# Optimization experiments

Hardware: AMD Instinct MI355X
Metric: run time of the kernel (lower is better)

## Reference

```python
import jax, jax.numpy as jnp
import numpy as np

B, T, D, H = 8, 2048, 1024, 128  # batch, seq (== block_size), n_embd, head_size


def setup_inputs() -> dict:
    key = jax.random.key(0)
    kx, kq, kk, kv = jax.random.split(key, 4)
    s = D ** -0.5  # rough linear-init scale
    return {
        "x": jax.random.normal(kx, (B, T, D), dtype=jnp.float32),
        "Wq": jax.random.normal(kq, (D, H), dtype=jnp.float32) * s,
        "Wk": jax.random.normal(kk, (D, H), dtype=jnp.float32) * s,
        "Wv": jax.random.normal(kv, (D, H), dtype=jnp.float32) * s,
    }


def reference(x, Wq, Wk, Wv):
    # Linear projections (no bias)
    q = x @ Wq  # [B, T, H]
    k = x @ Wk  # [B, T, H]
    v = x @ Wv  # [B, T, H]
    scale = k.shape[-1] ** -0.5
    scores = jnp.einsum("bth,bsh->bts", q, k) * scale  # [B, T, T]
    # causal mask from tril buffer
    causal = jnp.tril(jnp.ones((T, T), dtype=bool))
    scores = jnp.where(causal, scores, jnp.finfo(scores.dtype).min)
    att = jax.nn.softmax(scores, axis=-1)
    out = jnp.einsum("bts,bsh->bth", att, v)  # [B, T, H]
    return out
```

## Files before the change

kernel.cpp:

```cpp
#include <hip/hip_runtime.h>
#include <hip/hip_bf16.h>
#include <stdint.h>

typedef float f32x4 __attribute__((ext_vector_type(4)));
typedef __bf16 bf16x8 __attribute__((ext_vector_type(8)));

#define T_SEQ 2048
#define D_EMB 1024
#define H_DIM 128
#define NBATCH 8
#define NTOK 16384

typedef __attribute__((address_space(3))) uint32_t lds_u32;
typedef const __attribute__((address_space(1))) uint32_t glb_u32;

#define DPPF(x, ctrl)                                                    \
  __int_as_float(__builtin_amdgcn_update_dpp(                            \
      0, __float_as_int(x), (ctrl), 0xF, 0xF, true))

#define PIPE_FENCE()                                       \
  do {                                                     \
    asm volatile("s_waitcnt vmcnt(0)" ::: "memory");       \
    __builtin_amdgcn_s_barrier();                          \
    __builtin_amdgcn_sched_barrier(0);                     \
  } while (0)


__global__ __launch_bounds__(256) void prep_w_kernel(
    const float* __restrict__ Wq, const float* __restrict__ Wk,
    const float* __restrict__ Wv, __hip_bfloat16* __restrict__ Wt) {
  const int mat = blockIdx.x >> 7;
  const int h = blockIdx.x & 127;
  const float* W = (mat == 0) ? Wq : ((mat == 1) ? Wk : Wv);
  __hip_bfloat16* dst = Wt + (size_t)(mat * 128 + h) * D_EMB;
  for (int k = threadIdx.x; k < D_EMB; k += 256)
    dst[k] = __float2bfloat16(W[(size_t)k * H_DIM + h]);
}

__global__ __launch_bounds__(512) void proj_kernel(
    const float* __restrict__ x, const __hip_bfloat16* __restrict__ Wt,
    __hip_bfloat16* __restrict__ qb, __hip_bfloat16* __restrict__ kb,
    __hip_bfloat16* __restrict__ vt) {
  __shared__ __align__(16) float Af[2][64 * 64];
  __shared__ __align__(16) __hip_bfloat16 Bs[2][384 * 64];
  const int tid = threadIdx.x;
  const int wave = tid >> 6;
  const int lane = tid & 63;
  const int g = lane >> 4;
  const int lr = lane & 15;
  const int m0 = blockIdx.x * 64;
  const int wc = wave * 48;

  f32x4 acc[4][3];
#pragma unroll
  for (int m = 0; m < 4; ++m)
#pragma unroll
    for (int n = 0; n < 3; ++n) acc[m][n] = f32x4{0.f, 0.f, 0.f, 0.f};

  auto stageA = [&](int buf, int k0) {
#pragma unroll
    for (int i = 0; i < 2; ++i) {
      const int e = i * 512 + tid;
      const int row = e >> 4;
      const int un = e & 15;
      __builtin_amdgcn_global_load_lds(
          (glb_u32*)(uintptr_t)(x + (size_t)(m0 + row) * D_EMB + k0 +
                                ((un ^ (row & 15)) * 4)),
          (lds_u32*)(uintptr_t)(&Af[buf][e * 4]), 16, 0, 0);
    }
  };
  auto stageB = [&](int buf, int k0) {
#pragma unroll
    for (int i = 0; i < 6; ++i) {
      const int u = i * 512 + tid;
      const int row = u >> 3;
      const int chunk = u & 7;
      __builtin_amdgcn_global_load_lds(
          (glb_u32*)(uintptr_t)(Wt + (size_t)row * D_EMB + k0 +
                                ((chunk ^ (row & 7)) * 8)),
          (lds_u32*)(uintptr_t)(&Bs[buf][row * 64 + chunk * 8]), 16, 0, 0);
    }
  };
  auto compute = [&](int buf) {
#pragma unroll
    for (int kk = 0; kk < 2; ++kk) {
      bf16x8 a[4];
#pragma unroll
      for (int m = 0; m < 4; ++m) {
        const int row = m * 16 + lr;
        const int u0 = kk * 8 + g * 2;
        const f32x4 lo = *reinterpret_cast<const f32x4*>(
            &Af[buf][row * 64 + ((u0 ^ (row & 15)) * 4)]);
        const f32x4 hi = *reinterpret_cast<const f32x4*>(
            &Af[buf][row * 64 + (((u0 + 1) ^ (row & 15)) * 4)]);
        union { bf16x8 v; __hip_bfloat16 h[8]; } u;
        u.h[0] = __float2bfloat16(lo[0]);
        u.h[1] = __float2bfloat16(lo[1]);
        u.h[2] = __float2bfloat16(lo[2]);
        u.h[3] = __float2bfloat16(lo[3]);
        u.h[4] = __float2bfloat16(hi[0]);
        u.h[5] = __float2bfloat16(hi[1]);
        u.h[6] = __float2bfloat16(hi[2]);
        u.h[7] = __float2bfloat16(hi[3]);
        a[m] = u.v;
      }
#pragma unroll
      for (int n = 0; n < 3; ++n) {
        const int row = wc + n * 16 + lr;
        bf16x8 b = *reinterpret_cast<const bf16x8*>(
            &Bs[buf][row * 64 + (((kk * 4 + g) ^ (row & 7)) * 8)]);
#pragma unroll
        for (int m = 0; m < 4; ++m)
          acc[m][n] =
              __builtin_amdgcn_mfma_f32_16x16x32_bf16(a[m], b, acc[m][n], 0, 0, 0);
      }
    }
  };

  stageA(0, 0);
  stageB(0, 0);

  int cur = 0;
  for (int k = 0; k < 16; ++k) {
    PIPE_FENCE();
    if (k < 15) {
      stageA(cur ^ 1, (k + 1) * 64);
      stageB(cur ^ 1, (k + 1) * 64);
    }
    compute(cur);
    cur ^= 1;
  }

#pragma unroll
  for (int n = 0; n < 3; ++n) {
    const int ng = wc + n * 16 + lr;
    const int head = ng >> 7;
    const int h = ng & 127;
#pragma unroll
    for (int m = 0; m < 4; ++m) {
#pragma unroll
      for (int r = 0; r < 4; ++r) {
        const int row = m0 + m * 16 + g * 4 + r;
        const __hip_bfloat16 val = __float2bfloat16(acc[m][n][r]);
        if (head == 0) {
          qb[(size_t)row * H_DIM + h] = val;
        } else if (head == 1) {
          kb[(size_t)row * H_DIM + h] = val;
        } else {
          const int bi = row >> 11;
          const int t = row & (T_SEQ - 1);
          vt[((size_t)bi * H_DIM + h) * T_SEQ + t] = val;
        }
      }
    }
  }
}

__global__ __launch_bounds__(512) void attn_kernel(
    const __hip_bfloat16* __restrict__ qb, const __hip_bfloat16* __restrict__ kb,
    const __hip_bfloat16* __restrict__ vt, float* __restrict__ out,
    float* __restrict__ PA_O, float* __restrict__ PA_ml,
    float* __restrict__ PB_O, float* __restrict__ PB_ml) {
  __shared__ __align__(16) __hip_bfloat16 KV[2][16384];
  __shared__ __align__(16) __hip_bfloat16 Pl[8][16][40];
  __shared__ float Obuf[4][16][132];
  __shared__ float mbuf[8][16];
  __shared__ float lbuf[8][16];

  const int tid = threadIdx.x;
  const int wave = tid >> 6;
  const int lane = tid & 63;
  const int g = lane >> 4;
  const int lr = lane & 15;
  const int qt = wave >> 1;
  const int kp = wave & 1;
  const int idx = blockIdx.x;
  const int b = idx & 7;
  const int u = idx >> 3;

  const __hip_bfloat16* qB = qb + (size_t)b * T_SEQ * H_DIM;
  const __hip_bfloat16* kB = kb + (size_t)b * T_SEQ * H_DIM;
  const __hip_bfloat16* vB = vt + (size_t)b * H_DIM * T_SEQ;
  const float scale = 0.08838834764831845f;

  auto stage = [&](__hip_bfloat16* buf, int s0) {
#pragma unroll
    for (int i = 0; i < 2; ++i) {
      const int uu = tid + i * 512;
      const int row = uu >> 4, grp = uu & 15;
      __builtin_amdgcn_global_load_lds(
          (glb_u32*)(uintptr_t)(kB + (size_t)(s0 + row) * H_DIM +
                                ((grp ^ (row & 15)) * 8)),
          (lds_u32*)(uintptr_t)(buf + uu * 8), 16, 0, 0);
    }
#pragma unroll
    for (int i = 0; i < 2; ++i) {
      const int uu = tid + i * 512;
      const int h = uu >> 3, grp = uu & 7;
      __builtin_amdgcn_global_load_lds(
          (glb_u32*)(uintptr_t)(vB + (size_t)h * T_SEQ + s0 +
                                ((grp ^ (h & 7)) * 8)),
          (lds_u32*)(uintptr_t)(buf + 8192 + uu * 8), 16, 0, 0);
    }
  };

  auto process = [&](int tile, int rr0, int rr1, int mode) {
    const int qrow0 = tile * 64 + qt * 16;
    bf16x8 qf[4];
#pragma unroll
    for (int kt = 0; kt < 4; ++kt)
      qf[kt] = *reinterpret_cast<const bf16x8*>(
          qB + (size_t)(qrow0 + lr) * H_DIM + kt * 32 + g * 8);

    f32x4 oacc[8];
#pragma unroll
    for (int i = 0; i < 8; ++i) oacc[i] = f32x4{0.f, 0.f, 0.f, 0.f};
    float mrow[4] = {-1e30f, -1e30f, -1e30f, -1e30f};
    float lrow[4] = {0.f, 0.f, 0.f, 0.f};

    __hip_bfloat16* bufA = &KV[0][0];
    __hip_bfloat16* bufB = &KV[1][0];
    stage(bufA, rr0 * 64);

    for (int r = rr0; r <= rr1; ++r) {
      PIPE_FENCE();
      if (r < rr1) stage(bufB, (r + 1) * 64);
      const int s0 = r * 64;
      const bool active = (s0 + kp * 32) <= (qrow0 + 15);
      if (active) {
        f32x4 sacc[2];
        sacc[0] = f32x4{0.f, 0.f, 0.f, 0.f};
        sacc[1] = f32x4{0.f, 0.f, 0.f, 0.f};
#pragma unroll
        for (int nt = 0; nt < 2; ++nt) {
          const int kl = kp * 32 + nt * 16 + lr;
          const __hip_bfloat16* kr = bufA + kl * 128;
#pragma unroll
          for (int kt = 0; kt < 4; ++kt) {
            bf16x8 kf = *reinterpret_cast<const bf16x8*>(
                kr + (((kt * 4 + g) ^ (kl & 15)) * 8));
            sacc[nt] = __builtin_amdgcn_mfma_f32_16x16x32_bf16(qf[kt], kf,
                                                               sacc[nt], 0, 0, 0);
          }
        }
        bf16x8 vf[8];
#pragma unroll
        for (int ht = 0; ht < 8; ++ht) {
          const int h = ht * 16 + lr;
          vf[ht] = *reinterpret_cast<const bf16x8*>(
              bufA + 8192 + h * 64 + (((kp * 4 + g) ^ (h & 7)) * 8));
        }
        float sv[2][4];
#pragma unroll
        for (int nt = 0; nt < 2; ++nt)
#pragma unroll
          for (int rr = 0; rr < 4; ++rr) {
            const int key = s0 + kp * 32 + nt * 16 + lr;
            const int qr = qrow0 + g * 4 + rr;
            const float s = sacc[nt][rr] * scale;
            sv[nt][rr] = (key > qr) ? -1e30f : s;
          }
        float pm[4];
#pragma unroll
        for (int rr = 0; rr < 4; ++rr) pm[rr] = fmaxf(sv[0][rr], sv[1][rr]);
#pragma unroll
        for (int rr = 0; rr < 4; ++rr) {
          pm[rr] = fmaxf(pm[rr], DPPF(pm[rr], 0xB1));
          pm[rr] = fmaxf(pm[rr], DPPF(pm[rr], 0x4E));
          pm[rr] = fmaxf(pm[rr], DPPF(pm[rr], 0x141));
          pm[rr] = fmaxf(pm[rr], DPPF(pm[rr], 0x140));
        }
        bool ok = true;
#pragma unroll
        for (int rr = 0; rr < 4; ++rr) ok = ok && (pm[rr] <= mrow[rr] + 8.f);
        if (!__all((int)ok)) {
#pragma unroll
          for (int rr = 0; rr < 4; ++rr) {
            const float mnew = fmaxf(mrow[rr], pm[rr]);
            const float corr = __expf(mrow[rr] - mnew);
            mrow[rr] = mnew;
            lrow[rr] *= corr;
#pragma unroll
            for (int ht = 0; ht < 8; ++ht) oacc[ht][rr] *= corr;
          }
        }
        float rs[4];
#pragma unroll
        for (int rr = 0; rr < 4; ++rr) {
          const float p0 = __expf(sv[0][rr] - mrow[rr]);
          const float p1 = __expf(sv[1][rr] - mrow[rr]);
          Pl[wave][g * 4 + rr][lr] = __float2bfloat16(p0);
          Pl[wave][g * 4 + rr][16 + lr] = __float2bfloat16(p1);
          rs[rr] = p0 + p1;
        }
#pragma unroll
        for (int rr = 0; rr < 4; ++rr) {
          rs[rr] += DPPF(rs[rr], 0xB1);
          rs[rr] += DPPF(rs[rr], 0x4E);
          rs[rr] += DPPF(rs[rr], 0x141);
          rs[rr] += DPPF(rs[rr], 0x140);
        }
#pragma unroll
        for (int rr = 0; rr < 4; ++rr) lrow[rr] += rs[rr];
        bf16x8 pf = *reinterpret_cast<const bf16x8*>(&Pl[wave][lr][g * 8]);
#pragma unroll
        for (int ht = 0; ht < 8; ++ht)
          oacc[ht] = __builtin_amdgcn_mfma_f32_16x16x32_bf16(pf, vf[ht],
                                                             oacc[ht], 0, 0, 0);
      }
      __hip_bfloat16* t = bufA; bufA = bufB; bufB = t;
    }

    __syncthreads();
    if (kp == 1) {
#pragma unroll
      for (int ht = 0; ht < 8; ++ht)
#pragma unroll
        for (int rr = 0; rr < 4; ++rr)
          Obuf[qt][g * 4 + rr][ht * 16 + lr] = oacc[ht][rr];
      if (lr == 0) {
#pragma unroll
        for (int rr = 0; rr < 4; ++rr) {
          mbuf[wave][g * 4 + rr] = mrow[rr];
          lbuf[wave][g * 4 + rr] = lrow[rr];
        }
      }
    }
    __syncthreads();
    if (kp == 0) {
#pragma unroll
      for (int rr = 0; rr < 4; ++rr) {
        const float mB = mbuf[wave + 1][g * 4 + rr];
        const float lB = lbuf[wave + 1][g * 4 + rr];
        const float M = fmaxf(mrow[rr], mB);
        const float a = __expf(mrow[rr] - M);
        const float bt = __expf(mB - M);
        lrow[rr] = a * lrow[rr] + bt * lB;
        mrow[rr] = M;
#pragma unroll
        for (int ht = 0; ht < 8; ++ht)
          oacc[ht][rr] =
              a * oacc[ht][rr] + bt * Obuf[qt][g * 4 + rr][ht * 16 + lr];
      }
      if (mode == 0) {
#pragma unroll
        for (int ht = 0; ht < 8; ++ht)
#pragma unroll
          for (int rr = 0; rr < 4; ++rr) {
            const int qr = qrow0 + g * 4 + rr;
            out[((size_t)b * T_SEQ + qr) * H_DIM + ht * 16 + lr] =
                oacc[ht][rr] / lrow[rr];
          }
      } else {
        float* PO = (mode == 1) ? PA_O : PB_O;
        float* Pm = (mode == 1) ? PA_ml : PB_ml;
        const int slot = tile - 16;
#pragma unroll
        for (int rr = 0; rr < 4; ++rr) {
          const size_t pr = (size_t)(b * 16 + slot) * 64 + qt * 16 + g * 4 + rr;
#pragma unroll
          for (int ht = 0; ht < 8; ++ht)
            PO[pr * 128 + ht * 16 + lr] = oacc[ht][rr];
          if (lr == 0) {
            Pm[pr * 2 + 0] = mrow[rr];
            Pm[pr * 2 + 1] = lrow[rr];
          }
        }
      }
    }
    __syncthreads();
  };

  if (u < 16) {
    process(u, 0, u, 0);
    process(31 - u, 0, 15 - u, 1);
  } else {
    const int v = u - 16;
    process(31 - v, 16 - v, 31 - v, 2);
  }
}

__global__ __launch_bounds__(256) void combine_kernel(
    const float* __restrict__ PA_O, const float* __restrict__ PA_ml,
    const float* __restrict__ PB_O, const float* __restrict__ PB_ml,
    float* __restrict__ out) {
  const int b = blockIdx.x >> 4;
  const int s = blockIdx.x & 15;
  const int tid = threadIdx.x;
  const int row = tid >> 2;
  const int c0 = (tid & 3) * 32;
  const size_t pr = (size_t)(b * 16 + s) * 64 + row;
  const float mA = PA_ml[pr * 2], lA = PA_ml[pr * 2 + 1];
  const float mB = PB_ml[pr * 2], lB = PB_ml[pr * 2 + 1];
  const float M = fmaxf(mA, mB);
  const float a = __expf(mA - M), bb = __expf(mB - M);
  const float inv = 1.f / (a * lA + bb * lB);
  const float* oa = PA_O + pr * 128 + c0;
  const float* ob = PB_O + pr * 128 + c0;
  float* op = out + ((size_t)b * T_SEQ + (16 + s) * 64 + row) * H_DIM + c0;
#pragma unroll
  for (int i = 0; i < 32; i += 4) {
    const float4 x = *reinterpret_cast<const float4*>(oa + i);
    const float4 y = *reinterpret_cast<const float4*>(ob + i);
    float4 z;
    z.x = (a * x.x + bb * y.x) * inv;
    z.y = (a * x.y + bb * y.y) * inv;
    z.z = (a * x.z + bb * y.z) * inv;
    z.w = (a * x.w + bb * y.w) * inv;
    *reinterpret_cast<float4*>(op + i) = z;
  }
}

extern "C" void kernel_launch(void* const* d_in, const int* in_sizes, int n_in,
                              void* d_out, int out_size, void* d_ws, size_t ws_size,
                              hipStream_t stream) {
  const float* x = (const float*)d_in[0];
  const float* Wq = (const float*)d_in[1];
  const float* Wk = (const float*)d_in[2];
  const float* Wv = (const float*)d_in[3];
  float* out = (float*)d_out;

  __hip_bfloat16* Wt = (__hip_bfloat16*)d_ws;
  __hip_bfloat16* qbuf = Wt + (size_t)3 * 128 * 1024;
  __hip_bfloat16* kbuf = qbuf + (size_t)NTOK * H_DIM;
  __hip_bfloat16* vbuf = kbuf + (size_t)NTOK * H_DIM;
  float* fbase = (float*)(vbuf + (size_t)NBATCH * H_DIM * T_SEQ);
  float* PA_O = fbase;
  float* PA_ml = PA_O + (size_t)1048576;
  float* PB_O = PA_ml + 16384;
  float* PB_ml = PB_O + (size_t)1048576;

  hipLaunchKernelGGL(prep_w_kernel, dim3(384), dim3(256), 0, stream, Wq, Wk, Wv, Wt);
  hipLaunchKernelGGL(proj_kernel, dim3(256), dim3(512), 0, stream, x, Wt, qbuf,
                     kbuf, vbuf);
  hipLaunchKernelGGL(attn_kernel, dim3(256), dim3(512), 0, stream, qbuf, kbuf,
                     vbuf, out, PA_O, PA_ml, PB_O, PB_ml);
  hipLaunchKernelGGL(combine_kernel, dim3(128), dim3(256), 0, stream, PA_O,
                     PA_ml, PB_O, PB_ml, out);
}
```

Before: 70.63 us.

## Split every query tile's KV range into four chunks across a 1024-block grid

Attention work is redistributed so each of the 32 query tiles per batch gets its causal key range cut into four near-equal chunks, each handled by its own block (1024 blocks instead of 256). This replaces the previous pairing scheme and aims for finer load balance and more blocks in flight across the GPU. The combine kernel now merges four partial (O, m, l) results for every tile, not two for half the tiles. The O exchange buffer now reuses the KV shared memory to shrink LDS use. In exchange every output row goes through the fp32 partial buffer, which adds global traffic and combine work, and blocks with empty or tiny ranges add launch overhead.

```diff
diff --git a/kernel.cpp b/kernel.cpp
--- a/kernel.cpp
+++ b/kernel.cpp
@@ -158,14 +158,13 @@
 
 __global__ __launch_bounds__(512) void attn_kernel(
     const __hip_bfloat16* __restrict__ qb, const __hip_bfloat16* __restrict__ kb,
-    const __hip_bfloat16* __restrict__ vt, float* __restrict__ out,
-    float* __restrict__ PA_O, float* __restrict__ PA_ml,
-    float* __restrict__ PB_O, float* __restrict__ PB_ml) {
+    const __hip_bfloat16* __restrict__ vt,
+    float* __restrict__ PO, float* __restrict__ Pml) {
   __shared__ __align__(16) __hip_bfloat16 KV[2][16384];
   __shared__ __align__(16) __hip_bfloat16 Pl[8][16][40];
-  __shared__ float Obuf[4][16][132];
   __shared__ float mbuf[8][16];
   __shared__ float lbuf[8][16];
+  auto Obuf = reinterpret_cast<float(*)[16][132]>(&KV[0][0]);
 
   const int tid = threadIdx.x;
   const int wave = tid >> 6;
@@ -176,12 +175,17 @@
   const int kp = wave & 1;
   const int idx = blockIdx.x;
   const int b = idx & 7;
-  const int u = idx >> 3;
+  const int t = (idx >> 3) & 31;
+  const int j = idx >> 8;
+  const int n = t + 1;
+  const int r0 = (j * n) >> 2;
+  const int r1 = ((j + 1) * n) >> 2;
 
   const __hip_bfloat16* qB = qb + (size_t)b * T_SEQ * H_DIM;
   const __hip_bfloat16* kB = kb + (size_t)b * T_SEQ * H_DIM;
   const __hip_bfloat16* vB = vt + (size_t)b * H_DIM * T_SEQ;
   const float scale = 0.08838834764831845f;
+  const int qrow0 = t * 64 + qt * 16;
 
   auto stage = [&](__hip_bfloat16* buf, int s0) {
 #pragma unroll
@@ -204,210 +208,199 @@
     }
   };
 
-  auto process = [&](int tile, int rr0, int rr1, int mode) {
-    const int qrow0 = tile * 64 + qt * 16;
-    bf16x8 qf[4];
-#pragma unroll
-    for (int kt = 0; kt < 4; ++kt)
-      qf[kt] = *reinterpret_cast<const bf16x8*>(
-          qB + (size_t)(qrow0 + lr) * H_DIM + kt * 32 + g * 8);
-
-    f32x4 oacc[8];
-#pragma unroll
-    for (int i = 0; i < 8; ++i) oacc[i] = f32x4{0.f, 0.f, 0.f, 0.f};
-    float mrow[4] = {-1e30f, -1e30f, -1e30f, -1e30f};
-    float lrow[4] = {0.f, 0.f, 0.f, 0.f};
-
-    __hip_bfloat16* bufA = &KV[0][0];
-    __hip_bfloat16* bufB = &KV[1][0];
-    stage(bufA, rr0 * 64);
-
-    for (int r = rr0; r <= rr1; ++r) {
-      PIPE_FENCE();
-      if (r < rr1) stage(bufB, (r + 1) * 64);
-      const int s0 = r * 64;
-      const bool active = (s0 + kp * 32) <= (qrow0 + 15);
-      if (active) {
-        f32x4 sacc[2];
-        sacc[0] = f32x4{0.f, 0.f, 0.f, 0.f};
-        sacc[1] = f32x4{0.f, 0.f, 0.f, 0.f};
-#pragma unroll
-        for (int nt = 0; nt < 2; ++nt) {
-          const int kl = kp * 32 + nt * 16 + lr;
-          const __hip_bfloat16* kr = bufA + kl * 128;
-#pragma unroll
-          for (int kt = 0; kt < 4; ++kt) {
-            bf16x8 kf = *reinterpret_cast<const bf16x8*>(
-                kr + (((kt * 4 + g) ^ (kl & 15)) * 8));
-            sacc[nt] = __builtin_amdgcn_mfma_f32_16x16x32_bf16(qf[kt], kf,
-                                                               sacc[nt], 0, 0, 0);
-          }
+  bf16x8 qf[4];
+#pragma unroll
+  for (int kt = 0; kt < 4; ++kt)
+    qf[kt] = *reinterpret_cast<const bf16x8*>(
+        qB + (size_t)(qrow0 + lr) * H_DIM + kt * 32 + g * 8);
+
+  f32x4 oacc[8];
+#pragma unroll
+  for (int i = 0; i < 8; ++i) oacc[i] = f32x4{0.f, 0.f, 0.f, 0.f};
+  float mrow[4] = {-1e30f, -1e30f, -1e30f, -1e30f};
+  float lrow[4] = {0.f, 0.f, 0.f, 0.f};
+
+  __hip_bfloat16* bufA = &KV[0][0];
+  __hip_bfloat16* bufB = &KV[1][0];
+  if (r0 < r1) stage(bufA, r0 * 64);
+
+  for (int r = r0; r < r1; ++r) {
+    PIPE_FENCE();
+    if (r + 1 < r1) stage(bufB, (r + 1) * 64);
+    const int s0 = r * 64;
+    const bool active = (s0 + kp * 32) <= (qrow0 + 15);
+    if (active) {
+      f32x4 sacc[2];
+      sacc[0] = f32x4{0.f, 0.f, 0.f, 0.f};
+      sacc[1] = f32x4{0.f, 0.f, 0.f, 0.f};
+#pragma unroll
+      for (int nt = 0; nt < 2; ++nt) {
+        const int kl = kp * 32 + nt * 16 + lr;
+        const __hip_bfloat16* kr = bufA + kl * 128;
+#pragma unroll
+        for (int kt = 0; kt < 4; ++kt) {
+          bf16x8 kf = *reinterpret_cast<const bf16x8*>(
+              kr + (((kt * 4 + g) ^ (kl & 15)) * 8));
+          sacc[nt] = __builtin_amdgcn_mfma_f32_16x16x32_bf16(qf[kt], kf,
+                                                             sacc[nt], 0, 0, 0);
         }
-        bf16x8 vf[8];
-#pragma unroll
-        for (int ht = 0; ht < 8; ++ht) {
-          const int h = ht * 16 + lr;
-          vf[ht] = *reinterpret_cast<const bf16x8*>(
-              bufA + 8192 + h * 64 + (((kp * 4 + g) ^ (h & 7)) * 8));
+      }
+      bf16x8 vf[8];
+#pragma unroll
+      for (int ht = 0; ht < 8; ++ht) {
+        const int h = ht * 16 + lr;
+        vf[ht] = *reinterpret_cast<const bf16x8*>(
+            bufA + 8192 + h * 64 + (((kp * 4 + g) ^ (h & 7)) * 8));
+      }
+      float sv[2][4];
+#pragma unroll
+      for (int nt = 0; nt < 2; ++nt)
+#pragma unroll
+        for (int rr = 0; rr < 4; ++rr) {
+          const int key = s0 + kp * 32 + nt * 16 + lr;
+          const int qr = qrow0 + g * 4 + rr;
+          const float s = sacc[nt][rr] * scale;
+          sv[nt][rr] = (key > qr) ? -1e30f : s;
         }
-        float sv[2][4];
-#pragma unroll
-        for (int nt = 0; nt < 2; ++nt)
-#pragma unroll
-          for (int rr = 0; rr < 4; ++rr) {
-            const int key = s0 + kp * 32 + nt * 16 + lr;
-            const int qr = qrow0 + g * 4 + rr;
-            const float s = sacc[nt][rr] * scale;
-            sv[nt][rr] = (key > qr) ? -1e30f : s;
-          }
-        float pm[4];
-#pragma unroll
-        for (int rr = 0; rr < 4; ++rr) pm[rr] = fmaxf(sv[0][rr], sv[1][rr]);
+      float pm[4];
+#pragma unroll
+      for (int rr = 0; rr < 4; ++rr) pm[rr] = fmaxf(sv[0][rr], sv[1][rr]);
+#pragma unroll
+      for (int rr = 0; rr < 4; ++rr) {
+        pm[rr] = fmaxf(pm[rr], DPPF(pm[rr], 0xB1));
+        pm[rr] = fmaxf(pm[rr], DPPF(pm[rr], 0x4E));
+        pm[rr] = fmaxf(pm[rr], DPPF(pm[rr], 0x141));
+        pm[rr] = fmaxf(pm[rr], DPPF(pm[rr], 0x140));
+      }
+      bool ok = true;
+#pragma unroll
+      for (int rr = 0; rr < 4; ++rr) ok = ok && (pm[rr] <= mrow[rr] + 8.f);
+      if (!__all((int)ok)) {
 #pragma unroll
         for (int rr = 0; rr < 4; ++rr) {
-          pm[rr] = fmaxf(pm[rr], DPPF(pm[rr], 0xB1));
-          pm[rr] = fmaxf(pm[rr], DPPF(pm[rr], 0x4E));
-          pm[rr] = fmaxf(pm[rr], DPPF(pm[rr], 0x141));
-          pm[rr] = fmaxf(pm[rr], DPPF(pm[rr], 0x140));
+          const float mnew = fmaxf(mrow[rr], pm[rr]);
+          const float corr = __expf(mrow[rr] - mnew);
+          mrow[rr] = mnew;
+          lrow[rr] *= corr;
+#pragma unroll
+          for (int ht = 0; ht < 8; ++ht) oacc[ht][rr] *= corr;
         }
-        bool ok = true;
-#pragma unroll
-        for (int rr = 0; rr < 4; ++rr) ok = ok && (pm[rr] <= mrow[rr] + 8.f);
-        if (!__all((int)ok)) {
-#pragma unroll
-          for (int rr = 0; rr < 4; ++rr) {
-            const float mnew = fmaxf(mrow[rr], pm[rr]);
-            const float corr = __expf(mrow[rr] - mnew);
-            mrow[rr] = mnew;
-            lrow[rr] *= corr;
-#pragma unroll
-            for (int ht = 0; ht < 8; ++ht) oacc[ht][rr] *= corr;
-          }
-        }
-        float rs[4];
-#pragma unroll
-        for (int rr = 0; rr < 4; ++rr) {
-          const float p0 = __expf(sv[0][rr] - mrow[rr]);
-          const float p1 = __expf(sv[1][rr] - mrow[rr]);
-          Pl[wave][g * 4 + rr][lr] = __float2bfloat16(p0);
-          Pl[wave][g * 4 + rr][16 + lr] = __float2bfloat16(p1);
-          rs[rr] = p0 + p1;
-        }
-#pragma unroll
-        for (int rr = 0; rr < 4; ++rr) {
-          rs[rr] += DPPF(rs[rr], 0xB1);
-          rs[rr] += DPPF(rs[rr], 0x4E);
-          rs[rr] += DPPF(rs[rr], 0x141);
-          rs[rr] += DPPF(rs[rr], 0x140);
-        }
-#pragma unroll
-        for (int rr = 0; rr < 4; ++rr) lrow[rr] += rs[rr];
-        bf16x8 pf = *reinterpret_cast<const bf16x8*>(&Pl[wave][lr][g * 8]);
-#pragma unroll
-        for (int ht = 0; ht < 8; ++ht)
-          oacc[ht] = __builtin_amdgcn_mfma_f32_16x16x32_bf16(pf, vf[ht],
-                                                             oacc[ht], 0, 0, 0);
-      }
-      __hip_bfloat16* t = bufA; bufA = bufB; bufB = t;
-    }
-
-    __syncthreads();
-    if (kp == 1) {
+      }
+      float rs[4];
+#pragma unroll
+      for (int rr = 0; rr < 4; ++rr) {
+        const float p0 = __expf(sv[0][rr] - mrow[rr]);
+        const float p1 = __expf(sv[1][rr] - mrow[rr]);
+        Pl[wave][g * 4 + rr][lr] = __float2bfloat16(p0);
+        Pl[wave][g * 4 + rr][16 + lr] = __float2bfloat16(p1);
+        rs[rr] = p0 + p1;
+      }
+#pragma unroll
+      for (int rr = 0; rr < 4; ++rr) {
+        rs[rr] += DPPF(rs[rr], 0xB1);
+        rs[rr] += DPPF(rs[rr], 0x4E);
+        rs[rr] += DPPF(rs[rr], 0x141);
+        rs[rr] += DPPF(rs[rr], 0x140);
+      }
+#pragma unroll
+      for (int rr = 0; rr < 4; ++rr) lrow[rr] += rs[rr];
+      bf16x8 pf = *reinterpret_cast<const bf16x8*>(&Pl[wave][lr][g * 8]);
 #pragma unroll
       for (int ht = 0; ht < 8; ++ht)
-#pragma unroll
-        for (int rr = 0; rr < 4; ++rr)
-          Obuf[qt][g * 4 + rr][ht * 16 + lr] = oacc[ht][rr];
+        oacc[ht] = __builtin_amdgcn_mfma_f32_16x16x32_bf16(pf, vf[ht],
+                                                           oacc[ht], 0, 0, 0);
+    }
+    __hip_bfloat16* tmp = bufA; bufA = bufB; bufB = tmp;
+  }
+
+  __syncthreads();
+  if (kp == 1) {
+#pragma unroll
+    for (int ht = 0; ht < 8; ++ht)
+#pragma unroll
+      for (int rr = 0; rr < 4; ++rr)
+        Obuf[qt][g * 4 + rr][ht * 16 + lr] = oacc[ht][rr];
+    if (lr == 0) {
+#pragma unroll
+      for (int rr = 0; rr < 4; ++rr) {
+        mbuf[wave][g * 4 + rr] = mrow[rr];
+        lbuf[wave][g * 4 + rr] = lrow[rr];
+      }
+    }
+  }
+  __syncthreads();
+  if (kp == 0) {
+#pragma unroll
+    for (int rr = 0; rr < 4; ++rr) {
+      const float mB = mbuf[wave + 1][g * 4 + rr];
+      const float lB = lbuf[wave + 1][g * 4 + rr];
+      const float M = fmaxf(mrow[rr], mB);
+      const float a = __expf(mrow[rr] - M);
+      const float bt = __expf(mB - M);
+      lrow[rr] = a * lrow[rr] + bt * lB;
+      mrow[rr] = M;
+#pragma unroll
+      for (int ht = 0; ht < 8; ++ht)
+        oacc[ht][rr] =
+            a * oacc[ht][rr] + bt * Obuf[qt][g * 4 + rr][ht * 16 + lr];
+    }
+#pragma unroll
+    for (int rr = 0; rr < 4; ++rr) {
+      const size_t pr =
+          (((size_t)(b * 32 + t) * 4 + j) * 64) + qt * 16 + g * 4 + rr;
+#pragma unroll
+      for (int ht = 0; ht < 8; ++ht)
+        PO[pr * 128 + ht * 16 + lr] = oacc[ht][rr];
       if (lr == 0) {
-#pragma unroll
-        for (int rr = 0; rr < 4; ++rr) {
-          mbuf[wave][g * 4 + rr] = mrow[rr];
-          lbuf[wave][g * 4 + rr] = lrow[rr];
-        }
-      }
-    }
-    __syncthreads();
-    if (kp == 0) {
-#pragma unroll
-      for (int rr = 0; rr < 4; ++rr) {
-        const float mB = mbuf[wave + 1][g * 4 + rr];
-        const float lB = lbuf[wave + 1][g * 4 + rr];
-        const float M = fmaxf(mrow[rr], mB);
-        const float a = __expf(mrow[rr] - M);
-        const float bt = __expf(mB - M);
-        lrow[rr] = a * lrow[rr] + bt * lB;
-        mrow[rr] = M;
-#pragma unroll
-        for (int ht = 0; ht < 8; ++ht)
-          oacc[ht][rr] =
-              a * oacc[ht][rr] + bt * Obuf[qt][g * 4 + rr][ht * 16 + lr];
-      }
-      if (mode == 0) {
-#pragma unroll
-        for (int ht = 0; ht < 8; ++ht)
-#pragma unroll
-          for (int rr = 0; rr < 4; ++rr) {
-            const int qr = qrow0 + g * 4 + rr;
-            out[((size_t)b * T_SEQ + qr) * H_DIM + ht * 16 + lr] =
-                oacc[ht][rr] / lrow[rr];
-          }
-      } else {
-        float* PO = (mode == 1) ? PA_O : PB_O;
-        float* Pm = (mode == 1) ? PA_ml : PB_ml;
-        const int slot = tile - 16;
-#pragma unroll
-        for (int rr = 0; rr < 4; ++rr) {
-          const size_t pr = (size_t)(b * 16 + slot) * 64 + qt * 16 + g * 4 + rr;
-#pragma unroll
-          for (int ht = 0; ht < 8; ++ht)
-            PO[pr * 128 + ht * 16 + lr] = oacc[ht][rr];
-          if (lr == 0) {
-            Pm[pr * 2 + 0] = mrow[rr];
-            Pm[pr * 2 + 1] = lrow[rr];
-          }
-        }
-      }
-    }
-    __syncthreads();
-  };
-
-  if (u < 16) {
-    process(u, 0, u, 0);
-    process(31 - u, 0, 15 - u, 1);
-  } else {
-    const int v = u - 16;
-    process(31 - v, 16 - v, 31 - v, 2);
+        Pml[pr * 2 + 0] = mrow[rr];
+        Pml[pr * 2 + 1] = lrow[rr];
+      }
+    }
   }
 }
 
 __global__ __launch_bounds__(256) void combine_kernel(
-    const float* __restrict__ PA_O, const float* __restrict__ PA_ml,
-    const float* __restrict__ PB_O, const float* __restrict__ PB_ml,
+    const float* __restrict__ PO, const float* __restrict__ Pml,
     float* __restrict__ out) {
-  const int b = blockIdx.x >> 4;
-  const int s = blockIdx.x & 15;
+  const int b = blockIdx.x >> 5;
+  const int t = blockIdx.x & 31;
   const int tid = threadIdx.x;
   const int row = tid >> 2;
   const int c0 = (tid & 3) * 32;
-  const size_t pr = (size_t)(b * 16 + s) * 64 + row;
-  const float mA = PA_ml[pr * 2], lA = PA_ml[pr * 2 + 1];
-  const float mB = PB_ml[pr * 2], lB = PB_ml[pr * 2 + 1];
-  const float M = fmaxf(mA, mB);
-  const float a = __expf(mA - M), bb = __expf(mB - M);
-  const float inv = 1.f / (a * lA + bb * lB);
-  const float* oa = PA_O + pr * 128 + c0;
-  const float* ob = PB_O + pr * 128 + c0;
-  float* op = out + ((size_t)b * T_SEQ + (16 + s) * 64 + row) * H_DIM + c0;
+  const size_t base = (size_t)(b * 32 + t) * 4;
+
+  float m[4], l[4];
+#pragma unroll
+  for (int j = 0; j < 4; ++j) {
+    const size_t pr = (base + j) * 64 + row;
+    m[j] = Pml[pr * 2];
+    l[j] = Pml[pr * 2 + 1];
+  }
+  const float M = fmaxf(fmaxf(m[0], m[1]), fmaxf(m[2], m[3]));
+  float w[4];
+  float L = 0.f;
+#pragma unroll
+  for (int j = 0; j < 4; ++j) {
+    w[j] = __expf(m[j] - M);
+    L += w[j] * l[j];
+  }
+  const float inv = 1.f / L;
+
+  float* op = out + ((size_t)b * T_SEQ + t * 64 + row) * H_DIM + c0;
 #pragma unroll
   for (int i = 0; i < 32; i += 4) {
-    const float4 x = *reinterpret_cast<const float4*>(oa + i);
-    const float4 y = *reinterpret_cast<const float4*>(ob + i);
-    float4 z;
-    z.x = (a * x.x + bb * y.x) * inv;
-    z.y = (a * x.y + bb * y.y) * inv;
-    z.z = (a * x.z + bb * y.z) * inv;
-    z.w = (a * x.w + bb * y.w) * inv;
-    *reinterpret_cast<float4*>(op + i) = z;
+    float4 s = {0.f, 0.f, 0.f, 0.f};
+#pragma unroll
+    for (int j = 0; j < 4; ++j) {
+      const float4 v = *reinterpret_cast<const float4*>(
+          PO + ((base + j) * 64 + row) * 128 + c0 + i);
+      s.x += w[j] * v.x;
+      s.y += w[j] * v.y;
+      s.z += w[j] * v.z;
+      s.w += w[j] * v.w;
+    }
+    s.x *= inv; s.y *= inv; s.z *= inv; s.w *= inv;
+    *reinterpret_cast<float4*>(op + i) = s;
   }
 }
 
@@ -424,17 +417,14 @@
   __hip_bfloat16* qbuf = Wt + (size_t)3 * 128 * 1024;
   __hip_bfloat16* kbuf = qbuf + (size_t)NTOK * H_DIM;
   __hip_bfloat16* vbuf = kbuf + (size_t)NTOK * H_DIM;
-  float* fbase = (float*)(vbuf + (size_t)NBATCH * H_DIM * T_SEQ);
-  float* PA_O = fbase;
-  float* PA_ml = PA_O + (size_t)1048576;
-  float* PB_O = PA_ml + 16384;
-  float* PB_ml = PB_O + (size_t)1048576;
+  float* PO = (float*)(vbuf + (size_t)NBATCH * H_DIM * T_SEQ);
+  float* Pml = PO + (size_t)8 * 32 * 4 * 64 * 128;
 
   hipLaunchKernelGGL(prep_w_kernel, dim3(384), dim3(256), 0, stream, Wq, Wk, Wv, Wt);
   hipLaunchKernelGGL(proj_kernel, dim3(256), dim3(512), 0, stream, x, Wt, qbuf,
                      kbuf, vbuf);
-  hipLaunchKernelGGL(attn_kernel, dim3(256), dim3(512), 0, stream, qbuf, kbuf,
-                     vbuf, out, PA_O, PA_ml, PB_O, PB_ml);
-  hipLaunchKernelGGL(combine_kernel, dim3(128), dim3(256), 0, stream, PA_O,
-                     PA_ml, PB_O, PB_ml, out);
+  hipLaunchKernelGGL(attn_kernel, dim3(1024), dim3(512), 0, stream, qbuf, kbuf,
+                     vbuf, PO, Pml);
+  hipLaunchKernelGGL(combine_kernel, dim3(256), dim3(256), 0, stream, PO, Pml,
+                     out);
 }
```

After: 106.0 us. 50.1% more time.
